# Kernel optimization log

Hardware: AMD Instinct MI355X
Metric: run time of the kernel (lower is better)

## Reference

```python
import jax, jax.numpy as jnp
import numpy as np

N = 50000
HID = 128


def care_layer(h, src, dst, att_w, att_b, n_nodes):
    # att([x_i, x_j]) == x_i @ W[:H] + x_j @ W[H:]  (avoids materializing concat)
    H = h.shape[1]
    wi, wj = att_w[:H], att_w[H:]
    hi = h[dst]                                   # [E, H] gather (x_i = target)
    hj = h[src]                                   # [E, H] gather (x_j = source)
    alpha = jax.nn.sigmoid(hi @ wi + hj @ wj + att_b)  # [E, 1]
    msg = alpha * hj                              # [E, H]
    sums = jax.ops.segment_sum(msg, dst, num_segments=n_nodes)
    cnts = jax.ops.segment_sum(jnp.ones((src.shape[0],), h.dtype), dst, num_segments=n_nodes)
    return sums / jnp.maximum(cnts, 1.0)[:, None]  # scatter-mean; isolated nodes -> 0


def setup_inputs() -> dict:
    key = jax.random.key(0)
    ks = jax.random.split(key, 8)
    in_dim, hid, out_dim = 256, HID, 2
    x = jax.random.normal(ks[0], (N, in_dim), dtype=jnp.float32)
    edge_index = jax.random.randint(ks[1], (2, 1600000), 0, N, dtype=jnp.int64)
    s = lambda k, shp, fan: jax.random.normal(k, shp, jnp.float32) * (1.0 / np.sqrt(fan))
    return {
        "x": x,
        "edge_index": edge_index,
        "enc_w": s(ks[2], (in_dim, hid), in_dim),
        "enc_b": jnp.zeros((hid,), jnp.float32),
        "att1_w": s(ks[3], (2 * hid, 1), 2 * hid),
        "att1_b": jnp.zeros((1,), jnp.float32),
        "att2_w": s(ks[4], (2 * hid, 1), 2 * hid),
        "att2_b": jnp.zeros((1,), jnp.float32),
        "cls_w": s(ks[5], (hid, out_dim), hid),
        "cls_b": jnp.zeros((out_dim,), jnp.float32),
    }


def reference(x, edge_index, enc_w, enc_b, att1_w, att1_b, att2_w, att2_b, cls_w, cls_b):
    src, dst = edge_index[0], edge_index[1]  # PyG: x_j = x[src], aggregate at dst
    n = x.shape[0]
    h = jax.nn.relu(x @ enc_w + enc_b)       # dropout is identity in eval mode
    h = care_layer(h, src, dst, att1_w, att1_b, n)
    h = jax.nn.relu(h)
    h = care_layer(h, src, dst, att2_w, att2_b, n)
    return h @ cls_w + cls_b                 # [N, out_dim]
```

## Files before the change

### kernel.cpp

```cpp
#include <hip/hip_runtime.h>
#include <hip/hip_bf16.h>
#include <hip/hip_fp16.h>
#include <math.h>

#define HID 128
#define INDIM 256
#define CAP 6144
#define NBLK1 512

typedef _Float16 h2v __attribute__((ext_vector_type(2)));

#ifndef __has_builtin
#define __has_builtin(x) 0
#endif
#if __has_builtin(__builtin_amdgcn_fdot2)
#define FDOT2(a, b, c) __builtin_amdgcn_fdot2((a), (b), (c), false)
#else
__device__ __forceinline__ float FDOT2(h2v a, h2v b, float c) {
    return fmaf((float)a[0], (float)b[0], fmaf((float)a[1], (float)b[1], c));
}
#endif

__global__ void detect_i64_kernel(const int* __restrict__ idx32, int* __restrict__ flag) {
    int l = threadIdx.x;
    int v = idx32[2 * l + 1];
    unsigned long long ball = __ballot(v != 0);
    if (l == 0) flag[0] = (ball == 0ULL) ? 1 : 0;
}

__device__ __forceinline__ int load_src(const int* idx, int is64, int E, int e) {
    return is64 ? idx[2 * e] : idx[e];
}
__device__ __forceinline__ int load_dst(const int* idx, int is64, int E, int e) {
    return is64 ? idx[2 * (E + e)] : idx[E + e];
}

__global__ __launch_bounds__(256) void bucket_scatter_kernel(const int* __restrict__ idx32,
                                                             const int* __restrict__ flag,
                                                             int* __restrict__ bcursor,
                                                             unsigned int* __restrict__ recs,
                                                             int E, int NB) {
    __shared__ int hist[512];
    __shared__ int cur[512];
    int t = threadIdx.x;
    int CH = (E + NBLK1 - 1) / NBLK1;
    int e0 = blockIdx.x * CH;
    int e1 = min(e0 + CH, E);
    for (int i = t; i < NB; i += 256) hist[i] = 0;
    __syncthreads();
    int is64 = flag[0];
    for (int e = e0 + t; e < e1; e += 256) {
        int d = load_dst(idx32, is64, E, e);
        atomicAdd(&hist[d >> 7], 1);
    }
    __syncthreads();
    for (int i = t; i < NB; i += 256)
        cur[i] = atomicAdd(&bcursor[i], hist[i]);
    __syncthreads();
    for (int e = e0 + t; e < e1; e += 256) {
        int s = load_src(idx32, is64, E, e);
        int d = load_dst(idx32, is64, E, e);
        int b = d >> 7;
        int r = atomicAdd(&cur[b], 1);
        recs[(size_t)b * CAP + r] = ((unsigned)d << 16) | (unsigned)s;
    }
}

__global__ void bucket_scan_kernel(const int* __restrict__ bcursor,
                                   int* __restrict__ bbase, int NB) {
    int l = threadIdx.x;
    int i0 = l * 8;
    int v[8];
    #pragma unroll
    for (int k = 0; k < 8; k++) v[k] = (i0 + k < NB) ? bcursor[i0 + k] : 0;
    int s = 0;
    #pragma unroll
    for (int k = 0; k < 8; k++) s += v[k];
    int x = s;
    #pragma unroll
    for (int off = 1; off < 64; off <<= 1) {
        int y = __shfl_up(x, off);
        if (l >= off) x += y;
    }
    int run = x - s;
    #pragma unroll
    for (int k = 0; k < 8; k++) {
        if (i0 + k < NB) bbase[i0 + k] = run;
        run += v[k];
    }
}

__global__ __launch_bounds__(256) void csr_finalize_kernel(const unsigned int* __restrict__ recs,
                                                           const int* __restrict__ bcursor,
                                                           const int* __restrict__ bbase,
                                                           int* __restrict__ rowstart,
                                                           int* __restrict__ csr_src,
                                                           int N, int E) {
    __shared__ int h[128];
    __shared__ int ex[128];
    __shared__ int cu[128];
    int b = blockIdx.x;
    int t = threadIdx.x;
    int cnt = bcursor[b];
    int base = bbase[b];
    if (t < 128) h[t] = 0;
    __syncthreads();
    const unsigned int* r0 = recs + (size_t)b * CAP;
    for (int i = t; i < cnt; i += 256) {
        unsigned int rec = r0[i];
        atomicAdd(&h[(rec >> 16) & 127], 1);
    }
    __syncthreads();
    if (t < 64) {
        int a0 = h[2 * t], a1 = h[2 * t + 1];
        int s = a0 + a1;
        int x = s;
        #pragma unroll
        for (int off = 1; off < 64; off <<= 1) {
            int y = __shfl_up(x, off);
            if (t >= off) x += y;
        }
        ex[2 * t] = x - s;
        ex[2 * t + 1] = x - s + a0;
    }
    __syncthreads();
    int d0 = b * 128;
    if (t < 128) {
        if (d0 + t < N) rowstart[d0 + t] = base + ex[t];
        cu[t] = ex[t];
    }
    if (b == 0 && t == 0) rowstart[N] = E;
    __syncthreads();
    for (int i = t; i < cnt; i += 256) {
        unsigned int rec = r0[i];
        int dl = (rec >> 16) & 127;
        int r = atomicAdd(&cu[dl], 1);
        csr_src[base + r] = (int)(rec & 0xffffu);
    }
}

__global__ __launch_bounds__(256) void encoder_kernel(const float* __restrict__ x,
                                                      const float* __restrict__ W,
                                                      const float* __restrict__ b,
                                                      const float* __restrict__ attw,
                                                      const float* __restrict__ attb,
                                                      __half* __restrict__ h16,
                                                      float* __restrict__ ai,
                                                      float* __restrict__ aj, int N) {
    __shared__ h2v xsp[16][68];
    __shared__ h2v wspT[16][132];
    int t = threadIdx.x;
    int n0 = blockIdx.x * 64;
    int tc = t & 15, tr = t >> 4;
    int c0 = tc * 8, r0 = tr * 4;
    float acc[4][8];
    #pragma unroll
    for (int i = 0; i < 4; i++)
        #pragma unroll
        for (int j = 0; j < 8; j++) acc[i][j] = 0.f;

    int lr = t >> 2, lc4 = (t & 3) * 8;
    int wcg = t & 15, wk2 = t >> 4;

    for (int k0 = 0; k0 < INDIM; k0 += 32) {
        int gr = n0 + lr; if (gr >= N) gr = N - 1;
        const float4* xg = (const float4*)(x + (size_t)gr * INDIM + k0 + lc4);
        float4 a0 = xg[0], a1 = xg[1];
        int kb = lc4 >> 1;
        { h2v p; p[0] = (_Float16)a0.x; p[1] = (_Float16)a0.y; xsp[kb + 0][lr] = p; }
        { h2v p; p[0] = (_Float16)a0.z; p[1] = (_Float16)a0.w; xsp[kb + 1][lr] = p; }
        { h2v p; p[0] = (_Float16)a1.x; p[1] = (_Float16)a1.y; xsp[kb + 2][lr] = p; }
        { h2v p; p[0] = (_Float16)a1.z; p[1] = (_Float16)a1.w; xsp[kb + 3][lr] = p; }
        {
            const float4* w0 = (const float4*)(W + (size_t)(k0 + 2 * wk2) * HID + wcg * 8);
            const float4* w1 = (const float4*)(W + (size_t)(k0 + 2 * wk2 + 1) * HID + wcg * 8);
            float4 r0a = w0[0], r0b = w0[1];
            float4 r1a = w1[0], r1b = w1[1];
            union { float4 f; h2v h[4]; } ua, ub;
            ua.h[0][0] = (_Float16)r0a.x; ua.h[0][1] = (_Float16)r1a.x;
            ua.h[1][0] = (_Float16)r0a.y; ua.h[1][1] = (_Float16)r1a.y;
            ua.h[2][0] = (_Float16)r0a.z; ua.h[2][1] = (_Float16)r1a.z;
            ua.h[3][0] = (_Float16)r0a.w; ua.h[3][1] = (_Float16)r1a.w;
            ub.h[0][0] = (_Float16)r0b.x; ub.h[0][1] = (_Float16)r1b.x;
            ub.h[1][0] = (_Float16)r0b.y; ub.h[1][1] = (_Float16)r1b.y;
            ub.h[2][0] = (_Float16)r0b.z; ub.h[2][1] = (_Float16)r1b.z;
            ub.h[3][0] = (_Float16)r0b.w; ub.h[3][1] = (_Float16)r1b.w;
            *(float4*)&wspT[wcg][wk2 * 8]     = ua.f;
            *(float4*)&wspT[wcg][wk2 * 8 + 4] = ub.f;
        }
        __syncthreads();
        #pragma unroll
        for (int kk2 = 0; kk2 < 16; ++kk2) {
            union { float4 f; h2v h[4]; } ux, uw0, uw1;
            ux.f  = *(const float4*)&xsp[kk2][r0];
            uw0.f = *(const float4*)&wspT[tc][kk2 * 8];
            uw1.f = *(const float4*)&wspT[tc][kk2 * 8 + 4];
            #pragma unroll
            for (int i = 0; i < 4; i++) {
                #pragma unroll
                for (int j = 0; j < 4; j++) {
                    acc[i][j]     = FDOT2(ux.h[i], uw0.h[j], acc[i][j]);
                    acc[i][j + 4] = FDOT2(ux.h[i], uw1.h[j], acc[i][j + 4]);
                }
            }
        }
        __syncthreads();
    }
    float wiv[8], wjv[8];
    #pragma unroll
    for (int j = 0; j < 8; j++) { wiv[j] = attw[c0 + j]; wjv[j] = attw[HID + c0 + j]; }
    #pragma unroll
    for (int i = 0; i < 4; i++) {
        int gr = n0 + r0 + i;
        float ov[8];
        #pragma unroll
        for (int j = 0; j < 8; j++) {
            float o = acc[i][j] + b[c0 + j];
            ov[j] = o > 0.f ? o : 0.f;
        }
        if (gr < N) {
            union { float4 f; __half2 h[4]; } u;
            #pragma unroll
            for (int j = 0; j < 8; j += 2)
                u.h[j >> 1] = __float22half2_rn(make_float2(ov[j], ov[j + 1]));
            *(float4*)(h16 + (size_t)gr * HID + c0) = u.f;
        }
        float pi = 0.f, pj = 0.f;
        #pragma unroll
        for (int j = 0; j < 8; j++) { pi = fmaf(ov[j], wiv[j], pi); pj = fmaf(ov[j], wjv[j], pj); }
        #pragma unroll
        for (int off = 1; off < 16; off <<= 1) {
            pi += __shfl_xor(pi, off);
            pj += __shfl_xor(pj, off);
        }
        if (tc == 0 && gr < N) { ai[gr] = pi + attb[0]; aj[gr] = pj; }
    }
}

template <int MODE>
__global__ __launch_bounds__(256) void care_kernel(const __half* __restrict__ hh,
                                                   const float* __restrict__ ai,
                                                   const float* __restrict__ aj,
                                                   const int* __restrict__ rowstart,
                                                   const int* __restrict__ csr_src,
                                                   float* __restrict__ out,
                                                   __half* __restrict__ hh_out,
                                                   float* __restrict__ ai2,
                                                   float* __restrict__ aj2, int N,
                                                   const float* __restrict__ attw2,
                                                   const float* __restrict__ attb2,
                                                   const float* __restrict__ clsw,
                                                   const float* __restrict__ clsb) {
    int t = threadIdx.x;
    int lane = t & 63, w = t >> 6;
    int n = blockIdx.x * 4 + w;
    if (n >= N) return;
    int beg = rowstart[n], end = rowstart[n + 1];
    int deg = end - beg;
    float ain = ai[n];
    int g = lane >> 4;
    int r = lane & 15;

    float acc[8];
    #pragma unroll
    for (int k = 0; k < 8; k++) acc[k] = 0.f;

    const float4* hp = (const float4*)hh;
    for (int c0 = beg; c0 < end; c0 += 64) {
        int m = end - c0; if (m > 64) m = 64;
        int li = lane < m ? lane : m - 1;
        int sl = csr_src[c0 + li];
        float ajl = aj[sl];
        float al = 1.0f / (1.0f + __expf(-(ain + ajl)));
        if (lane >= m) al = 0.f;
        int nit = (m + 3) >> 2;
        #pragma unroll 4
        for (int it = 0; it < nit; ++it) {
            int idx = it * 4 + g;
            float a = __shfl(al, idx);
            int s = __shfl(sl, idx);
            float4 hv = hp[(size_t)s * 16 + r];
            union { float4 f; __half2 h[4]; } u; u.f = hv;
            #pragma unroll
            for (int k = 0; k < 4; k++) {
                float2 fv = __half22float2(u.h[k]);
                acc[2 * k + 0] = fmaf(a, fv.x, acc[2 * k + 0]);
                acc[2 * k + 1] = fmaf(a, fv.y, acc[2 * k + 1]);
            }
        }
    }
    #pragma unroll
    for (int k = 0; k < 8; k++) {
        acc[k] += __shfl_xor(acc[k], 16);
        acc[k] += __shfl_xor(acc[k], 32);
    }
    float scale = 1.0f / fmaxf((float)deg, 1.0f);

    if (MODE == 0) {
        float mv[8];
        #pragma unroll
        for (int k = 0; k < 8; k++) {
            float o = acc[k] * scale;
            mv[k] = o > 0.f ? o : 0.f;
        }
        if (g == 0) {
            union { float4 f; __half2 h[4]; } u;
            #pragma unroll
            for (int k = 0; k < 4; k++)
                u.h[k] = __float22half2_rn(make_float2(mv[2 * k], mv[2 * k + 1]));
            ((float4*)hh_out)[(size_t)n * 16 + r] = u.f;
        }
        float pi = 0.f, pj = 0.f;
        #pragma unroll
        for (int k = 0; k < 8; k++) {
            int f = r * 8 + k;
            pi = fmaf(mv[k], attw2[f], pi);
            pj = fmaf(mv[k], attw2[HID + f], pj);
        }
        #pragma unroll
        for (int off = 1; off < 16; off <<= 1) {
            pi += __shfl_xor(pi, off);
            pj += __shfl_xor(pj, off);
        }
        if (lane == 0) { ai2[n] = pi + attb2[0]; aj2[n] = pj; }
    } else {
        float p0 = 0.f, p1 = 0.f;
        #pragma unroll
        for (int k = 0; k < 8; k++) {
            float m = acc[k] * scale;
            int f = r * 8 + k;
            p0 = fmaf(m, clsw[f * 2 + 0], p0);
            p1 = fmaf(m, clsw[f * 2 + 1], p1);
        }
        #pragma unroll
        for (int off = 8; off >= 1; off >>= 1) {
            p0 += __shfl_xor(p0, off);
            p1 += __shfl_xor(p1, off);
        }
        if (lane == 0) {
            out[(size_t)n * 2 + 0] = p0 + clsb[0];
            out[(size_t)n * 2 + 1] = p1 + clsb[1];
        }
    }
}

extern "C" void kernel_launch(void* const* d_in, const int* in_sizes, int n_in,
                              void* d_out, int out_size, void* d_ws, size_t ws_size,
                              hipStream_t stream) {
    const float* x      = (const float*)d_in[0];
    const int*   idx32  = (const int*)d_in[1];
    const float* enc_w  = (const float*)d_in[2];
    const float* enc_b  = (const float*)d_in[3];
    const float* att1_w = (const float*)d_in[4];
    const float* att1_b = (const float*)d_in[5];
    const float* att2_w = (const float*)d_in[6];
    const float* att2_b = (const float*)d_in[7];
    const float* cls_w  = (const float*)d_in[8];
    const float* cls_b  = (const float*)d_in[9];
    float* out = (float*)d_out;

    int N = in_sizes[0] / INDIM;
    int E = in_sizes[1] / 2;
    int NB = (N + 127) >> 7;

    char* p = (char*)d_ws;
    __half* h16a = (__half*)p; p += (size_t)N * HID * 2;
    __half* h16b = (__half*)p; p += (size_t)N * HID * 2;
    int* csr_src  = (int*)p; p += (size_t)E * 4;
    unsigned int* recs = (unsigned int*)p; p += (size_t)NB * CAP * 4;
    float* ai   = (float*)p; p += (size_t)N * 4;
    float* aj   = (float*)p; p += (size_t)N * 4;
    float* ai2  = (float*)p; p += (size_t)N * 4;
    float* aj2  = (float*)p; p += (size_t)N * 4;
    int* rowstart = (int*)p; p += (size_t)(N + 1) * 4;
    int* bcursor  = (int*)p; p += (size_t)NB * 4;
    int* bbase    = (int*)p; p += (size_t)NB * 4;
    int* flag     = (int*)p; p += 64;

    hipMemsetAsync(bcursor, 0, (size_t)NB * 4, stream);
    detect_i64_kernel<<<1, 64, 0, stream>>>(idx32, flag);
    bucket_scatter_kernel<<<NBLK1, 256, 0, stream>>>(idx32, flag, bcursor, recs, E, NB);
    bucket_scan_kernel<<<1, 64, 0, stream>>>(bcursor, bbase, NB);
    csr_finalize_kernel<<<NB, 256, 0, stream>>>(recs, bcursor, bbase, rowstart,
                                                csr_src, N, E);

    encoder_kernel<<<(N + 63) / 64, 256, 0, stream>>>(x, enc_w, enc_b, att1_w, att1_b,
                                                      h16a, ai, aj, N);

    care_kernel<0><<<(N + 3) / 4, 256, 0, stream>>>(h16a, ai, aj, rowstart, csr_src,
                                                    nullptr, h16b, ai2, aj2, N,
                                                    att2_w, att2_b, nullptr, nullptr);
    care_kernel<1><<<(N + 3) / 4, 256, 0, stream>>>(h16b, ai2, aj2, rowstart, csr_src,
                                                    out, nullptr, nullptr, nullptr, N,
                                                    nullptr, nullptr, cls_w, cls_b);
}
```

Before: 293.5 us.

## Split care aggregation across four feature-chunk blocks with partial-sum combine kernels

```diff
diff --git a/kernel.cpp b/kernel.cpp
--- a/kernel.cpp
+++ b/kernel.cpp
@@ -238,48 +238,50 @@
 }
 
 template <int MODE>
-__global__ __launch_bounds__(256) void care_kernel(const __half* __restrict__ hh,
-                                                   const float* __restrict__ ai,
-                                                   const float* __restrict__ aj,
-                                                   const int* __restrict__ rowstart,
-                                                   const int* __restrict__ csr_src,
-                                                   float* __restrict__ out,
-                                                   __half* __restrict__ hh_out,
-                                                   float* __restrict__ ai2,
-                                                   float* __restrict__ aj2, int N,
-                                                   const float* __restrict__ attw2,
-                                                   const float* __restrict__ attb2,
-                                                   const float* __restrict__ clsw,
-                                                   const float* __restrict__ clsb) {
+__global__ __launch_bounds__(256) void care2_kernel(const __half* __restrict__ hh,
+                                                    const float* __restrict__ ai,
+                                                    const float* __restrict__ aj,
+                                                    const int* __restrict__ rowstart,
+                                                    const int* __restrict__ csr_src,
+                                                    __half* __restrict__ hh_out,
+                                                    float* __restrict__ aip,
+                                                    float* __restrict__ ajp,
+                                                    float* __restrict__ outp, int N,
+                                                    const float* __restrict__ attw2,
+                                                    const float* __restrict__ clsw) {
+    int b = blockIdx.x;
+    int c = b & 3;
+    int m = b >> 2;
     int t = threadIdx.x;
     int lane = t & 63, w = t >> 6;
-    int n = blockIdx.x * 4 + w;
+    int n = m * 4 + w;
     if (n >= N) return;
     int beg = rowstart[n], end = rowstart[n + 1];
     int deg = end - beg;
     float ain = ai[n];
-    int g = lane >> 4;
-    int r = lane & 15;
+    int es = lane >> 2;
+    int fl = lane & 3;
 
     float acc[8];
     #pragma unroll
     for (int k = 0; k < 8; k++) acc[k] = 0.f;
 
     const float4* hp = (const float4*)hh;
+    int fofs = c * 4 + fl;
     for (int c0 = beg; c0 < end; c0 += 64) {
-        int m = end - c0; if (m > 64) m = 64;
-        int li = lane < m ? lane : m - 1;
+        int mm = end - c0; if (mm > 64) mm = 64;
+        int li = lane < mm ? lane : mm - 1;
         int sl = csr_src[c0 + li];
         float ajl = aj[sl];
         float al = 1.0f / (1.0f + __expf(-(ain + ajl)));
-        if (lane >= m) al = 0.f;
-        int nit = (m + 3) >> 2;
+        if (lane >= mm) al = 0.f;
+        int nit = (mm + 15) >> 4;
         #pragma unroll 4
         for (int it = 0; it < nit; ++it) {
-            int idx = it * 4 + g;
+            int idx = it * 16 + es;
             float a = __shfl(al, idx);
             int s = __shfl(sl, idx);
-            float4 hv = hp[(size_t)s * 16 + r];
+            float4 hv = hp[(size_t)s * 16 + fofs];
             union { float4 f; __half2 h[4]; } u; u.f = hv;
             #pragma unroll
             for (int k = 0; k < 4; k++) {
@@ -291,6 +293,8 @@
     }
     #pragma unroll
     for (int k = 0; k < 8; k++) {
+        acc[k] += __shfl_xor(acc[k], 4);
+        acc[k] += __shfl_xor(acc[k], 8);
         acc[k] += __shfl_xor(acc[k], 16);
         acc[k] += __shfl_xor(acc[k], 32);
     }
@@ -303,45 +307,65 @@
             float o = acc[k] * scale;
             mv[k] = o > 0.f ? o : 0.f;
         }
-        if (g == 0) {
+        if (es == 0) {
             union { float4 f; __half2 h[4]; } u;
             #pragma unroll
             for (int k = 0; k < 4; k++)
                 u.h[k] = __float22half2_rn(make_float2(mv[2 * k], mv[2 * k + 1]));
-            ((float4*)hh_out)[(size_t)n * 16 + r] = u.f;
+            ((float4*)hh_out)[(size_t)n * 16 + fofs] = u.f;
         }
         float pi = 0.f, pj = 0.f;
         #pragma unroll
         for (int k = 0; k < 8; k++) {
-            int f = r * 8 + k;
+            int f = c * 32 + fl * 8 + k;
             pi = fmaf(mv[k], attw2[f], pi);
             pj = fmaf(mv[k], attw2[HID + f], pj);
         }
-        #pragma unroll
-        for (int off = 1; off < 16; off <<= 1) {
-            pi += __shfl_xor(pi, off);
-            pj += __shfl_xor(pj, off);
-        }
-        if (lane == 0) { ai2[n] = pi + attb2[0]; aj2[n] = pj; }
+        pi += __shfl_xor(pi, 1); pi += __shfl_xor(pi, 2);
+        pj += __shfl_xor(pj, 1); pj += __shfl_xor(pj, 2);
+        if (lane == 0) { aip[(size_t)c * N + n] = pi; ajp[(size_t)c * N + n] = pj; }
     } else {
         float p0 = 0.f, p1 = 0.f;
         #pragma unroll
         for (int k = 0; k < 8; k++) {
-            float m = acc[k] * scale;
-            int f = r * 8 + k;
-            p0 = fmaf(m, clsw[f * 2 + 0], p0);
-            p1 = fmaf(m, clsw[f * 2 + 1], p1);
-        }
-        #pragma unroll
-        for (int off = 8; off >= 1; off >>= 1) {
-            p0 += __shfl_xor(p0, off);
-            p1 += __shfl_xor(p1, off);
-        }
+            float mvv = acc[k] * scale;
+            int f = c * 32 + fl * 8 + k;
+            p0 = fmaf(mvv, clsw[f * 2 + 0], p0);
+            p1 = fmaf(mvv, clsw[f * 2 + 1], p1);
+        }
+        p0 += __shfl_xor(p0, 1); p0 += __shfl_xor(p0, 2);
+        p1 += __shfl_xor(p1, 1); p1 += __shfl_xor(p1, 2);
         if (lane == 0) {
-            out[(size_t)n * 2 + 0] = p0 + clsb[0];
-            out[(size_t)n * 2 + 1] = p1 + clsb[1];
-        }
-    }
+            outp[((size_t)c * N + n) * 2 + 0] = p0;
+            outp[((size_t)c * N + n) * 2 + 1] = p1;
+        }
+    }
+}
+
+__global__ __launch_bounds__(256) void combine_att_kernel(const float* __restrict__ aip,
+                                                          const float* __restrict__ ajp,
+                                                          const float* __restrict__ attb2,
+                                                          float* __restrict__ ai2,
+                                                          float* __restrict__ aj2, int N) {
+    int i = blockIdx.x * 256 + threadIdx.x;
+    if (i >= N) return;
+    ai2[i] = aip[i] + aip[(size_t)N + i] + aip[2 * (size_t)N + i] + aip[3 * (size_t)N + i] + attb2[0];
+    aj2[i] = ajp[i] + ajp[(size_t)N + i] + ajp[2 * (size_t)N + i] + ajp[3 * (size_t)N + i];
+}
+
+__global__ __launch_bounds__(256) void combine_out_kernel(const float* __restrict__ outp,
+                                                          const float* __restrict__ clsb,
+                                                          float* __restrict__ out, int N) {
+    int i = blockIdx.x * 256 + threadIdx.x;
+    if (i >= N) return;
+    float o0 = 0.f, o1 = 0.f;
+    #pragma unroll
+    for (int cc = 0; cc < 4; cc++) {
+        o0 += outp[((size_t)cc * N + i) * 2 + 0];
+        o1 += outp[((size_t)cc * N + i) * 2 + 1];
+    }
+    out[(size_t)i * 2 + 0] = o0 + clsb[0];
+    out[(size_t)i * 2 + 1] = o1 + clsb[1];
 }
 
 extern "C" void kernel_launch(void* const* d_in, const int* in_sizes, int n_in,
@@ -362,6 +386,7 @@
     int N = in_sizes[0] / INDIM;
     int E = in_sizes[1] / 2;
     int NB = (N + 127) >> 7;
+    int G4 = ((N + 3) / 4) * 4;
 
     char* p = (char*)d_ws;
     __half* h16a = (__half*)p; p += (size_t)N * HID * 2;
@@ -372,6 +397,9 @@
     float* aj   = (float*)p; p += (size_t)N * 4;
     float* ai2  = (float*)p; p += (size_t)N * 4;
     float* aj2  = (float*)p; p += (size_t)N * 4;
+    float* aip  = (float*)p; p += (size_t)4 * N * 4;
+    float* ajp  = (float*)p; p += (size_t)4 * N * 4;
+    float* outp = (float*)p; p += (size_t)4 * N * 2 * 4;
     int* rowstart = (int*)p; p += (size_t)(N + 1) * 4;
     int* bcursor  = (int*)p; p += (size_t)NB * 4;
     int* bbase    = (int*)p; p += (size_t)NB * 4;
@@ -387,10 +415,11 @@
     encoder_kernel<<<(N + 63) / 64, 256, 0, stream>>>(x, enc_w, enc_b, att1_w, att1_b,
                                                       h16a, ai, aj, N);
 
-    care_kernel<0><<<(N + 3) / 4, 256, 0, stream>>>(h16a, ai, aj, rowstart, csr_src,
-                                                    nullptr, h16b, ai2, aj2, N,
-                                                    att2_w, att2_b, nullptr, nullptr);
-    care_kernel<1><<<(N + 3) / 4, 256, 0, stream>>>(h16b, ai2, aj2, rowstart, csr_src,
-                                                    out, nullptr, nullptr, nullptr, N,
-                                                    nullptr, nullptr, cls_w, cls_b);
-}
+    care2_kernel<0><<<G4, 256, 0, stream>>>(h16a, ai, aj, rowstart, csr_src,
+                                            h16b, aip, ajp, nullptr, N, att2_w, nullptr);
+    combine_att_kernel<<<(N + 255) / 256, 256, 0, stream>>>(aip, ajp, att2_b, ai2, aj2, N);
+    care2_kernel<1><<<G4, 256, 0, stream>>>(h16b, ai2, aj2, rowstart, csr_src,
+                                            nullptr, nullptr, nullptr, outp, N,
+                                            nullptr, cls_w);
+    combine_out_kernel<<<(N + 255) / 256, 256, 0, stream>>>(outp, cls_b, out, N);
+}
```

Measured after the change: 401.5 us. 1.37x slower.

## Fuse encoder and edge bucket scatter into one launch; fold scan into finalize

Applied to the files above, without the earlier changes.

```diff
diff --git a/kernel.cpp b/kernel.cpp
--- a/kernel.cpp
+++ b/kernel.cpp
@@ -35,121 +35,46 @@
     return is64 ? idx[2 * (E + e)] : idx[E + e];
 }
 
-__global__ __launch_bounds__(256) void bucket_scatter_kernel(const int* __restrict__ idx32,
-                                                             const int* __restrict__ flag,
-                                                             int* __restrict__ bcursor,
-                                                             unsigned int* __restrict__ recs,
-                                                             int E, int NB) {
-    __shared__ int hist[512];
-    __shared__ int cur[512];
+__global__ __launch_bounds__(256) void enc_scatter_kernel(
+        const float* __restrict__ x, const float* __restrict__ W,
+        const float* __restrict__ b, const float* __restrict__ attw,
+        const float* __restrict__ attb, __half* __restrict__ h16,
+        float* __restrict__ ai, float* __restrict__ aj, int N, int EBenc,
+        const int* __restrict__ idx32, const int* __restrict__ flag,
+        int* __restrict__ bcursor, unsigned int* __restrict__ recs, int E, int NB) {
+    __shared__ __align__(16) char smem[12800];
     int t = threadIdx.x;
-    int CH = (E + NBLK1 - 1) / NBLK1;
-    int e0 = blockIdx.x * CH;
-    int e1 = min(e0 + CH, E);
-    for (int i = t; i < NB; i += 256) hist[i] = 0;
-    __syncthreads();
-    int is64 = flag[0];
-    for (int e = e0 + t; e < e1; e += 256) {
-        int d = load_dst(idx32, is64, E, e);
-        atomicAdd(&hist[d >> 7], 1);
-    }
-    __syncthreads();
-    for (int i = t; i < NB; i += 256)
-        cur[i] = atomicAdd(&bcursor[i], hist[i]);
-    __syncthreads();
-    for (int e = e0 + t; e < e1; e += 256) {
-        int s = load_src(idx32, is64, E, e);
-        int d = load_dst(idx32, is64, E, e);
-        int b = d >> 7;
-        int r = atomicAdd(&cur[b], 1);
-        recs[(size_t)b * CAP + r] = ((unsigned)d << 16) | (unsigned)s;
-    }
-}
-
-__global__ void bucket_scan_kernel(const int* __restrict__ bcursor,
-                                   int* __restrict__ bbase, int NB) {
-    int l = threadIdx.x;
-    int i0 = l * 8;
-    int v[8];
-    #pragma unroll
-    for (int k = 0; k < 8; k++) v[k] = (i0 + k < NB) ? bcursor[i0 + k] : 0;
-    int s = 0;
-    #pragma unroll
-    for (int k = 0; k < 8; k++) s += v[k];
-    int x = s;
-    #pragma unroll
-    for (int off = 1; off < 64; off <<= 1) {
-        int y = __shfl_up(x, off);
-        if (l >= off) x += y;
-    }
-    int run = x - s;
-    #pragma unroll
-    for (int k = 0; k < 8; k++) {
-        if (i0 + k < NB) bbase[i0 + k] = run;
-        run += v[k];
-    }
-}
-
-__global__ __launch_bounds__(256) void csr_finalize_kernel(const unsigned int* __restrict__ recs,
-                                                           const int* __restrict__ bcursor,
-                                                           const int* __restrict__ bbase,
-                                                           int* __restrict__ rowstart,
-                                                           int* __restrict__ csr_src,
-                                                           int N, int E) {
-    __shared__ int h[128];
-    __shared__ int ex[128];
-    __shared__ int cu[128];
-    int b = blockIdx.x;
-    int t = threadIdx.x;
-    int cnt = bcursor[b];
-    int base = bbase[b];
-    if (t < 128) h[t] = 0;
-    __syncthreads();
-    const unsigned int* r0 = recs + (size_t)b * CAP;
-    for (int i = t; i < cnt; i += 256) {
-        unsigned int rec = r0[i];
-        atomicAdd(&h[(rec >> 16) & 127], 1);
-    }
-    __syncthreads();
-    if (t < 64) {
-        int a0 = h[2 * t], a1 = h[2 * t + 1];
-        int s = a0 + a1;
-        int x = s;
-        #pragma unroll
-        for (int off = 1; off < 64; off <<= 1) {
-            int y = __shfl_up(x, off);
-            if (t >= off) x += y;
-        }
-        ex[2 * t] = x - s;
-        ex[2 * t + 1] = x - s + a0;
-    }
-    __syncthreads();
-    int d0 = b * 128;
-    if (t < 128) {
-        if (d0 + t < N) rowstart[d0 + t] = base + ex[t];
-        cu[t] = ex[t];
-    }
-    if (b == 0 && t == 0) rowstart[N] = E;
-    __syncthreads();
-    for (int i = t; i < cnt; i += 256) {
-        unsigned int rec = r0[i];
-        int dl = (rec >> 16) & 127;
-        int r = atomicAdd(&cu[dl], 1);
-        csr_src[base + r] = (int)(rec & 0xffffu);
-    }
-}
-
-__global__ __launch_bounds__(256) void encoder_kernel(const float* __restrict__ x,
-                                                      const float* __restrict__ W,
-                                                      const float* __restrict__ b,
-                                                      const float* __restrict__ attw,
-                                                      const float* __restrict__ attb,
-                                                      __half* __restrict__ h16,
-                                                      float* __restrict__ ai,
-                                                      float* __restrict__ aj, int N) {
-    __shared__ h2v xsp[16][68];
-    __shared__ h2v wspT[16][132];
-    int t = threadIdx.x;
+
+    if ((int)blockIdx.x >= EBenc) {
+        int* hist = (int*)smem;
+        int* cur  = (int*)(smem + 2048);
+        int sbid = blockIdx.x - EBenc;
+        int CH = (E + NBLK1 - 1) / NBLK1;
+        int e0 = sbid * CH;
+        int e1 = min(e0 + CH, E);
+        for (int i = t; i < NB; i += 256) hist[i] = 0;
+        __syncthreads();
+        int is64 = flag[0];
+        for (int e = e0 + t; e < e1; e += 256) {
+            int d = load_dst(idx32, is64, E, e);
+            atomicAdd(&hist[d >> 7], 1);
+        }
+        __syncthreads();
+        for (int i = t; i < NB; i += 256)
+            cur[i] = atomicAdd(&bcursor[i], hist[i]);
+        __syncthreads();
+        for (int e = e0 + t; e < e1; e += 256) {
+            int s = load_src(idx32, is64, E, e);
+            int d = load_dst(idx32, is64, E, e);
+            int bb = d >> 7;
+            int r = atomicAdd(&cur[bb], 1);
+            recs[(size_t)bb * CAP + r] = ((unsigned)d << 16) | (unsigned)s;
+        }
+        return;
+    }
+
+    h2v (*xsp)[68]  = (h2v(*)[68])smem;
+    h2v (*wspT)[132] = (h2v(*)[132])(smem + 4352);
     int n0 = blockIdx.x * 64;
     int tc = t & 15, tr = t >> 4;
     int c0 = tc * 8, r0 = tr * 4;
@@ -237,6 +162,61 @@
     }
 }
 
+__global__ __launch_bounds__(256) void csr_finalize_kernel(const unsigned int* __restrict__ recs,
+                                                           const int* __restrict__ bcursor,
+                                                           int* __restrict__ rowstart,
+                                                           int* __restrict__ csr_src,
+                                                           int N, int E) {
+    __shared__ int h[128];
+    __shared__ int ex[128];
+    __shared__ int cu[128];
+    __shared__ int wred[4];
+    int b = blockIdx.x;
+    int t = threadIdx.x;
+    int lane = t & 63, w = t >> 6;
+    int partial = 0;
+    for (int i = t; i < b; i += 256) partial += bcursor[i];
+    #pragma unroll
+    for (int off = 32; off >= 1; off >>= 1) partial += __shfl_xor(partial, off);
+    if (lane == 0) wred[w] = partial;
+    if (t < 128) h[t] = 0;
+    __syncthreads();
+    int base = wred[0] + wred[1] + wred[2] + wred[3];
+    int cnt = bcursor[b];
+    const unsigned int* r0 = recs + (size_t)b * CAP;
+    for (int i = t; i < cnt; i += 256) {
+        unsigned int rec = r0[i];
+        atomicAdd(&h[(rec >> 16) & 127], 1);
+    }
+    __syncthreads();
+    if (t < 64) {
+        int a0 = h[2 * t], a1 = h[2 * t + 1];
+        int s = a0 + a1;
+        int x = s;
+        #pragma unroll
+        for (int off = 1; off < 64; off <<= 1) {
+            int y = __shfl_up(x, off);
+            if (t >= off) x += y;
+        }
+        ex[2 * t] = x - s;
+        ex[2 * t + 1] = x - s + a0;
+    }
+    __syncthreads();
+    int d0 = b * 128;
+    if (t < 128) {
+        if (d0 + t < N) rowstart[d0 + t] = base + ex[t];
+        cu[t] = ex[t];
+    }
+    if (b == 0 && t == 0) rowstart[N] = E;
+    __syncthreads();
+    for (int i = t; i < cnt; i += 256) {
+        unsigned int rec = r0[i];
+        int dl = (rec >> 16) & 127;
+        int r = atomicAdd(&cu[dl], 1);
+        csr_src[base + r] = (int)(rec & 0xffffu);
+    }
+}
+
 template <int MODE>
 __global__ __launch_bounds__(256) void care_kernel(const __half* __restrict__ hh,
                                                    const float* __restrict__ ai,
@@ -362,6 +342,7 @@
     int N = in_sizes[0] / INDIM;
     int E = in_sizes[1] / 2;
     int NB = (N + 127) >> 7;
+    int EBenc = (N + 63) / 64;
 
     char* p = (char*)d_ws;
     __half* h16a = (__half*)p; p += (size_t)N * HID * 2;
@@ -374,18 +355,14 @@
     float* aj2  = (float*)p; p += (size_t)N * 4;
     int* rowstart = (int*)p; p += (size_t)(N + 1) * 4;
     int* bcursor  = (int*)p; p += (size_t)NB * 4;
-    int* bbase    = (int*)p; p += (size_t)NB * 4;
     int* flag     = (int*)p; p += 64;
 
     hipMemsetAsync(bcursor, 0, (size_t)NB * 4, stream);
     detect_i64_kernel<<<1, 64, 0, stream>>>(idx32, flag);
-    bucket_scatter_kernel<<<NBLK1, 256, 0, stream>>>(idx32, flag, bcursor, recs, E, NB);
-    bucket_scan_kernel<<<1, 64, 0, stream>>>(bcursor, bbase, NB);
-    csr_finalize_kernel<<<NB, 256, 0, stream>>>(recs, bcursor, bbase, rowstart,
-                                                csr_src, N, E);
-
-    encoder_kernel<<<(N + 63) / 64, 256, 0, stream>>>(x, enc_w, enc_b, att1_w, att1_b,
-                                                      h16a, ai, aj, N);
+    enc_scatter_kernel<<<EBenc + NBLK1, 256, 0, stream>>>(x, enc_w, enc_b, att1_w, att1_b,
+                                                          h16a, ai, aj, N, EBenc,
+                                                          idx32, flag, bcursor, recs, E, NB);
+    csr_finalize_kernel<<<NB, 256, 0, stream>>>(recs, bcursor, rowstart, csr_src, N, E);
 
     care_kernel<0><<<(N + 3) / 4, 256, 0, stream>>>(h16a, ai, aj, rowstart, csr_src,
                                                     nullptr, h16b, ai2, aj2, N,
```

Result: faster. 266.5 us (-9.2%).
